# Performance work log

Hardware: AMD Instinct MI355X
Metric: run time of the kernel (lower is better)

## Reference

```python
import jax, jax.numpy as jnp
import numpy as np

N_USER, N_SPOT, D = 100000, 50000, 128
E_VISIT, E_REV, E_NEAR = 500000, 500000, 200000
P_DROP = 0.1


def _glorot(k, fan_in, fan_out):
    lim = jnp.sqrt(6.0 / (fan_in + fan_out))
    return jax.random.uniform(k, (fan_in, fan_out), jnp.float32, -lim, lim)


def setup_inputs() -> dict:
    key = jax.random.key(0)
    ks = jax.random.split(key, 14)
    return {
        "x_user": jax.random.normal(ks[0], (N_USER, D), jnp.float32),
        "x_spot": jax.random.normal(ks[1], (N_SPOT, D), jnp.float32),
        "W_visit_src": _glorot(ks[2], D, D),   # user side of (user,visit,spot)
        "W_visit_tgt": _glorot(ks[3], D, D),   # spot side of (user,visit,spot)
        "W_rev_src": _glorot(ks[4], D, D),     # spot side of (spot,visited_by,user)
        "W_rev_tgt": _glorot(ks[5], D, D),     # user side of (spot,visited_by,user)
        "W_near_src": _glorot(ks[6], D, D),    # (spot,near,spot)
        "W_near_tgt": _glorot(ks[7], D, D),
        "visit_src": jax.random.randint(ks[8], (E_VISIT,), 0, N_USER, jnp.int64),
        "visit_dst": jax.random.randint(ks[9], (E_VISIT,), 0, N_SPOT, jnp.int64),
        "rev_src": jax.random.randint(ks[10], (E_REV,), 0, N_SPOT, jnp.int64),
        "rev_dst": jax.random.randint(ks[11], (E_REV,), 0, N_USER, jnp.int64),
        "near_src": jax.random.randint(ks[12], (E_NEAR,), 0, N_SPOT, jnp.int64),
        "near_dst": jax.random.randint(ks[13], (E_NEAR,), 0, N_SPOT, jnp.int64),
    }


def _scatter_mean(vals, idx, n_seg):
    # scatter(..., reduce='mean') into zeros: empty segments stay 0
    s = jax.ops.segment_sum(vals, idx, num_segments=n_seg)
    c = jax.ops.segment_sum(jnp.ones((vals.shape[0],), vals.dtype), idx, num_segments=n_seg)
    return s / jnp.maximum(c, 1.0)[:, None]


def _edge_type(x_src, x_tgt, W_src, W_tgt, src_idx, dst_idx, n_tgt, dkey):
    src_p = x_src @ W_src                      # [N_src, D]
    tgt_p = x_tgt @ W_tgt                      # [N_tgt, D]
    g = src_p[src_idx]                         # gather per edge [E, D]
    keep = jax.random.bernoulli(dkey, 1.0 - P_DROP, g.shape)
    g = jnp.where(keep, g / (1.0 - P_DROP), jnp.zeros_like(g))  # dropout (training)
    return tgt_p + _scatter_mean(g, dst_idx, n_tgt)


def reference(x_user, x_spot, W_visit_src, W_visit_tgt, W_rev_src, W_rev_tgt,
              W_near_src, W_near_tgt, visit_src, visit_dst, rev_src, rev_dst,
              near_src, near_dst):
    dk = jax.random.key(1)
    spot_a = _edge_type(x_user, x_spot, W_visit_src, W_visit_tgt,
                        visit_src, visit_dst, N_SPOT, jax.random.fold_in(dk, 0))
    user_a = _edge_type(x_spot, x_user, W_rev_src, W_rev_tgt,
                        rev_src, rev_dst, N_USER, jax.random.fold_in(dk, 1))
    spot_b = _edge_type(x_spot, x_spot, W_near_src, W_near_tgt,
                        near_src, near_dst, N_SPOT, jax.random.fold_in(dk, 2))
    # div: spot receives from 2 edge types, user from 1
    out_user = jax.nn.relu(user_a / 1.0)
    out_spot = jax.nn.relu((spot_a + spot_b) / 2.0)
    # ReLU=True applies a second relu (no-op after the first, kept for faithfulness)
    return jax.nn.relu(out_user), jax.nn.relu(out_spot)
```

## Files before the change

### kernel.cpp

```cpp
#include <hip/hip_runtime.h>
#include <stdint.h>

#define DF 128
typedef unsigned short ushort_t;
typedef __attribute__((ext_vector_type(8))) short short8v;
typedef __attribute__((ext_vector_type(4))) float f32x4;

__host__ __device__ __forceinline__ unsigned rotl32(unsigned v, int r) {
  return __builtin_rotateleft32(v, (unsigned)r);
}

__host__ __device__ __forceinline__ void threefry2x32(
    unsigned k0, unsigned k1, unsigned c0, unsigned c1,
    unsigned& o0, unsigned& o1) {
  unsigned kx = k0 ^ k1 ^ 0x1BD11BDAu;
  unsigned x0 = c0 + k0;
  unsigned x1 = c1 + k1;
#define TF_R(r) { x0 += x1; x1 = rotl32(x1, r); x1 ^= x0; }
  TF_R(13) TF_R(15) TF_R(26) TF_R(6)
  x0 += k1; x1 += kx + 1u;
  TF_R(17) TF_R(29) TF_R(16) TF_R(24)
  x0 += kx; x1 += k0 + 2u;
  TF_R(13) TF_R(15) TF_R(26) TF_R(6)
  x0 += k0; x1 += k1 + 3u;
  TF_R(17) TF_R(29) TF_R(16) TF_R(24)
  x0 += k1; x1 += kx + 4u;
  TF_R(13) TF_R(15) TF_R(26) TF_R(6)
  x0 += kx; x1 += k0 + 5u;
#undef TF_R
  o0 = x0; o1 = x1;
}

#define KEEP_THR 0xE6666600u

__device__ __forceinline__ ushort_t f2bf(float f) {
  unsigned u = __float_as_uint(f);
  unsigned r = (u + 0x7fffu + ((u >> 16) & 1u)) >> 16;
  return (ushort_t)r;
}
__device__ __forceinline__ float bf2f(ushort_t h) {
  return __uint_as_float(((unsigned)h) << 16);
}

template <int EPI>
__global__ __launch_bounds__(256) void gemm_mfma(
    const float* __restrict__ X, const float* __restrict__ W1,
    const float* __restrict__ W2, int M,
    ushort_t* __restrict__ outB, float* __restrict__ outF,
    const ushort_t* __restrict__ m1, const ushort_t* __restrict__ m2) {
  __shared__ ushort_t Wt[DF][136];
  const int t = threadIdx.x;
  const int lane = t & 63;
  const int w = t >> 6;
  const int lr = lane & 15;
  const int kg = lane >> 4;
  const int rbase = blockIdx.x * 128;

#pragma unroll
  for (int i = 0; i < 16; ++i) {
    int q = t + i * 256;
    int k = q >> 5;
    int c4 = (q & 31) * 4;
    float4 wv = *reinterpret_cast<const float4*>(&W1[k * DF + c4]);
    if constexpr (EPI == 2) {
      float4 w2 = *reinterpret_cast<const float4*>(&W2[k * DF + c4]);
      wv.x += w2.x; wv.y += w2.y; wv.z += w2.z; wv.w += w2.w;
    }
    Wt[c4 + 0][k] = f2bf(wv.x);
    Wt[c4 + 1][k] = f2bf(wv.y);
    Wt[c4 + 2][k] = f2bf(wv.z);
    Wt[c4 + 3][k] = f2bf(wv.w);
  }
  __syncthreads();

  f32x4 acc[2][8];
#pragma unroll
  for (int rg = 0; rg < 2; ++rg)
#pragma unroll
    for (int n = 0; n < 8; ++n) acc[rg][n] = (f32x4){0.f, 0.f, 0.f, 0.f};

#pragma unroll
  for (int kt = 0; kt < 4; ++kt) {
    const int kb = kt * 32 + kg * 8;
    short8v a[2];
#pragma unroll
    for (int rg = 0; rg < 2; ++rg) {
      int r = rbase + w * 32 + rg * 16 + lr;
      float4 x0 = make_float4(0.f, 0.f, 0.f, 0.f);
      float4 x1 = x0;
      if (r < M) {
        x0 = *reinterpret_cast<const float4*>(&X[(size_t)r * DF + kb]);
        x1 = *reinterpret_cast<const float4*>(&X[(size_t)r * DF + kb + 4]);
      }
      short8v av;
      av[0] = (short)f2bf(x0.x); av[1] = (short)f2bf(x0.y);
      av[2] = (short)f2bf(x0.z); av[3] = (short)f2bf(x0.w);
      av[4] = (short)f2bf(x1.x); av[5] = (short)f2bf(x1.y);
      av[6] = (short)f2bf(x1.z); av[7] = (short)f2bf(x1.w);
      a[rg] = av;
    }
#pragma unroll
    for (int n = 0; n < 8; ++n) {
      short8v b = *reinterpret_cast<const short8v*>(&Wt[n * 16 + lr][kb]);
#pragma unroll
      for (int rg = 0; rg < 2; ++rg)
        acc[rg][n] = __builtin_amdgcn_mfma_f32_16x16x32_bf16(a[rg], b, acc[rg][n], 0, 0, 0);
    }
  }

#pragma unroll
  for (int rg = 0; rg < 2; ++rg) {
    const int rb = rbase + w * 32 + rg * 16 + kg * 4;
#pragma unroll
    for (int n = 0; n < 8; ++n) {
      const int col = n * 16 + lr;
#pragma unroll
      for (int j = 0; j < 4; ++j) {
        const int r = rb + j;
        if (r < M) {
          float vv = acc[rg][n][j];
          if (EPI == 0) {
            outB[(size_t)r * DF + col] = f2bf(vv);
          } else if (EPI == 1) {
            outF[(size_t)r * DF + col] =
                fmaxf(vv + bf2f(m1[(size_t)r * DF + col]), 0.f);
          } else {
            outF[(size_t)r * DF + col] =
                fmaxf(0.5f * (vv + bf2f(m1[(size_t)r * DF + col])
                                 + bf2f(m2[(size_t)r * DF + col])), 0.f);
          }
        }
      }
    }
  }
}

__global__ __launch_bounds__(256) void hist3(
    const int* __restrict__ vd, const int* __restrict__ rd,
    const int* __restrict__ nd, unsigned* __restrict__ deg_all,
    int Ev, int Er, int En, int segU, int segN) {
  int i = blockIdx.x * 256 + threadIdx.x;
  if (i < Ev) atomicAdd(&deg_all[vd[i]], 1u);
  else if (i < Ev + Er) atomicAdd(&deg_all[segU + rd[i - Ev]], 1u);
  else if (i < Ev + Er + En) atomicAdd(&deg_all[segN + nd[i - Ev - Er]], 1u);
}

#define SCAN_E 2048

__global__ __launch_bounds__(256) void scanA(
    const unsigned* __restrict__ deg, unsigned* __restrict__ bsum, int NT) {
  __shared__ unsigned sm[256];
  const int t = threadIdx.x;
  const int base = blockIdx.x * SCAN_E + t * 8;
  unsigned s = 0;
#pragma unroll
  for (int j = 0; j < 8; ++j) {
    int i = base + j;
    s += (i < NT) ? deg[i] : 0u;
  }
  sm[t] = s;
  __syncthreads();
  for (int off = 128; off; off >>= 1) {
    if (t < off) sm[t] += sm[t + off];
    __syncthreads();
  }
  if (t == 0) bsum[blockIdx.x] = sm[0];
}

__global__ __launch_bounds__(1024) void scanB(
    unsigned* __restrict__ bsum, unsigned* __restrict__ rp_all,
    int nb, int NT) {
  __shared__ unsigned sm[1024];
  const int t = threadIdx.x;
  unsigned v = (t < nb) ? bsum[t] : 0u;
  sm[t] = v;
  __syncthreads();
  for (int off = 1; off < 1024; off <<= 1) {
    unsigned u = (t >= off) ? sm[t - off] : 0u;
    __syncthreads();
    sm[t] += u;
    __syncthreads();
  }
  if (t < nb) bsum[t] = sm[t] - v;
  if (t == nb - 1) rp_all[NT] = sm[t];
}

__global__ __launch_bounds__(256) void scanC(
    const unsigned* __restrict__ deg, const unsigned* __restrict__ bsum,
    unsigned* __restrict__ rp, unsigned* __restrict__ cur, int NT) {
  __shared__ unsigned sm[256];
  const int t = threadIdx.x;
  const int base = blockIdx.x * SCAN_E + t * 8;
  unsigned vals[8];
  unsigned s = 0;
#pragma unroll
  for (int j = 0; j < 8; ++j) {
    int i = base + j;
    vals[j] = (i < NT) ? deg[i] : 0u;
    s += vals[j];
  }
  sm[t] = s;
  __syncthreads();
  for (int off = 1; off < 256; off <<= 1) {
    unsigned u = (t >= off) ? sm[t - off] : 0u;
    __syncthreads();
    sm[t] += u;
    __syncthreads();
  }
  unsigned run = bsum[blockIdx.x] + sm[t] - s;
#pragma unroll
  for (int j = 0; j < 8; ++j) {
    int i = base + j;
    if (i < NT) { rp[i] = run; cur[i] = run; }
    run += vals[j];
  }
}

__global__ __launch_bounds__(256) void fill3(
    const int* __restrict__ vs, const int* __restrict__ vd,
    const int* __restrict__ rs, const int* __restrict__ rd,
    const int* __restrict__ ns, const int* __restrict__ nd,
    unsigned* __restrict__ cur_all, uint2* __restrict__ es_all,
    int Ev, int Er, int En, int segU, int segN) {
  int i = blockIdx.x * 256 + threadIdx.x;
  if (i < Ev) {
    unsigned slot = atomicAdd(&cur_all[vd[i]], 1u);
    es_all[slot] = make_uint2((unsigned)i, (unsigned)vs[i]);
  } else if (i < Ev + Er) {
    int e = i - Ev;
    unsigned slot = atomicAdd(&cur_all[segU + rd[e]], 1u);
    es_all[slot] = make_uint2((unsigned)e, (unsigned)rs[e]);
  } else if (i < Ev + Er + En) {
    int e = i - Ev - Er;
    unsigned slot = atomicAdd(&cur_all[segN + nd[e]], 1u);
    es_all[slot] = make_uint2((unsigned)e, (unsigned)ns[e]);
  }
}

__global__ __launch_bounds__(256) void gather_reduce(
    const ushort_t* __restrict__ proj, const uint2* __restrict__ es,
    const unsigned* __restrict__ rowptr, ushort_t* __restrict__ accum,
    int ndst, unsigned emax, unsigned k0, unsigned k1) {
  const int lane = threadIdx.x & 63;
  int d = blockIdx.x * 4 + (threadIdx.x >> 6);
  d = __builtin_amdgcn_readfirstlane(d);
  if (d >= ndst) return;
  const unsigned b0 = __builtin_amdgcn_readfirstlane(rowptr[d]);
  const unsigned n  = __builtin_amdgcn_readfirstlane(rowptr[d + 1]) - b0;

  const unsigned lane2 = (unsigned)lane * 2u;

  uint2 e0 = es[min(b0, emax)];
  uint2 e1 = es[min(b0 + 1u, emax)];
  unsigned g0 =
      reinterpret_cast<const unsigned*>(proj + ((size_t)e0.y << 7))[lane];

  float a0 = 0.f, a1 = 0.f;
  for (unsigned i = 0; i < n; ++i) {
    const unsigned g = g0;
    const unsigned eid = e0.x;
    g0 = reinterpret_cast<const unsigned*>(proj + ((size_t)e1.y << 7))[lane];
    e0 = e1;
    e1 = es[min(b0 + i + 2u, emax)];

    const unsigned cb = eid * 128u + lane2;
    unsigned r0, r1, q0, q1;
    threefry2x32(k0, k1, 0u, cb, r0, r1);
    threefry2x32(k0, k1, 0u, cb + 1u, q0, q1);
    const float m0 = ((r0 ^ r1) < KEEP_THR) ? (1.0f / 0.9f) : 0.f;
    const float m1 = ((q0 ^ q1) < KEEP_THR) ? (1.0f / 0.9f) : 0.f;
    a0 = fmaf(__uint_as_float(g << 16), m0, a0);
    a1 = fmaf(__uint_as_float(g & 0xffff0000u), m1, a1);
  }

  const float inv = 1.0f / fmaxf((float)n, 1.0f);
  const unsigned pk =
      ((unsigned)f2bf(a0 * inv)) | (((unsigned)f2bf(a1 * inv)) << 16);
  reinterpret_cast<unsigned*>(accum)[(size_t)d * 64 + lane] = pk;
}

extern "C" void kernel_launch(void* const* d_in, const int* in_sizes, int n_in,
                              void* d_out, int out_size, void* d_ws, size_t ws_size,
                              hipStream_t stream) {
  const float* x_user      = (const float*)d_in[0];
  const float* x_spot      = (const float*)d_in[1];
  const float* W_visit_src = (const float*)d_in[2];
  const float* W_visit_tgt = (const float*)d_in[3];
  const float* W_rev_src   = (const float*)d_in[4];
  const float* W_rev_tgt   = (const float*)d_in[5];
  const float* W_near_src  = (const float*)d_in[6];
  const float* W_near_tgt  = (const float*)d_in[7];
  const int* visit_src = (const int*)d_in[8];
  const int* visit_dst = (const int*)d_in[9];
  const int* rev_src   = (const int*)d_in[10];
  const int* rev_dst   = (const int*)d_in[11];
  const int* near_src  = (const int*)d_in[12];
  const int* near_dst  = (const int*)d_in[13];

  const int n_user = in_sizes[0] / DF;
  const int n_spot = in_sizes[1] / DF;
  const int e_visit = in_sizes[8];
  const int e_rev   = in_sizes[10];
  const int e_near  = in_sizes[12];

  float* out_user = (float*)d_out;
  float* out_spot = out_user + (size_t)n_user * DF;

  const int NT = n_spot + n_user + n_spot;
  const int segU = n_spot;
  const int segN = n_spot + n_user;
  const int etot = e_visit + e_rev + e_near;
  const unsigned emax = (unsigned)(etot - 1);

  char* ws = (char*)d_ws;
  size_t off = 0;
  auto alloc = [&](size_t bytes) -> void* {
    void* p = ws + off;
    off += (bytes + 255) & ~(size_t)255;
    return p;
  };
  ushort_t* proj_vs  = (ushort_t*)alloc((size_t)n_user * DF * 2);
  ushort_t* proj_rs  = (ushort_t*)alloc((size_t)n_spot * DF * 2);
  ushort_t* proj_ns  = (ushort_t*)alloc((size_t)n_spot * DF * 2);
  ushort_t* accum_sv = (ushort_t*)alloc((size_t)n_spot * DF * 2);
  ushort_t* accum_u  = (ushort_t*)alloc((size_t)n_user * DF * 2);
  ushort_t* accum_sn = (ushort_t*)alloc((size_t)n_spot * DF * 2);
  uint2*    es_all   = (uint2*)   alloc((size_t)etot * 8);
  unsigned* rp_all   = (unsigned*)alloc(((size_t)NT + 1) * 4);
  unsigned* cur_all  = (unsigned*)alloc((size_t)NT * 4);
  unsigned* deg_all  = (unsigned*)alloc((size_t)NT * 4);
  unsigned* bsum     = (unsigned*)alloc(4096);

  unsigned kv0, kv1, kr0, kr1, kn0, kn1;
  threefry2x32(0u, 1u, 0u, 0u, kv0, kv1);
  threefry2x32(0u, 1u, 0u, 1u, kr0, kr1);
  threefry2x32(0u, 1u, 0u, 2u, kn0, kn1);

  dim3 blk(256);
  const int gb_user = (n_user + 127) / 128;
  const int gb_spot = (n_spot + 127) / 128;
  const int gb_e = (etot + 255) / 256;
  const int nb_scan = (NT + SCAN_E - 1) / SCAN_E;

  hipMemsetAsync(deg_all, 0, (size_t)NT * 4, stream);
  hist3<<<gb_e, blk, 0, stream>>>(visit_dst, rev_dst, near_dst, deg_all,
                                  e_visit, e_rev, e_near, segU, segN);
  scanA<<<nb_scan, blk, 0, stream>>>(deg_all, bsum, NT);
  scanB<<<1, 1024, 0, stream>>>(bsum, rp_all, nb_scan, NT);
  scanC<<<nb_scan, blk, 0, stream>>>(deg_all, bsum, rp_all, cur_all, NT);
  fill3<<<gb_e, blk, 0, stream>>>(visit_src, visit_dst, rev_src, rev_dst,
                                  near_src, near_dst, cur_all, es_all,
                                  e_visit, e_rev, e_near, segU, segN);

  gemm_mfma<0><<<gb_user, blk, 0, stream>>>(x_user, W_visit_src, nullptr, n_user,
                                            proj_vs, nullptr, nullptr, nullptr);
  gemm_mfma<0><<<gb_spot, blk, 0, stream>>>(x_spot, W_rev_src, nullptr, n_spot,
                                            proj_rs, nullptr, nullptr, nullptr);
  gemm_mfma<0><<<gb_spot, blk, 0, stream>>>(x_spot, W_near_src, nullptr, n_spot,
                                            proj_ns, nullptr, nullptr, nullptr);

  gather_reduce<<<(n_spot + 3) / 4, blk, 0, stream>>>(
      proj_vs, es_all, rp_all, accum_sv, n_spot, emax, kv0, kv1);
  gather_reduce<<<(n_user + 3) / 4, blk, 0, stream>>>(
      proj_rs, es_all, rp_all + segU, accum_u, n_user, emax, kr0, kr1);
  gather_reduce<<<(n_spot + 3) / 4, blk, 0, stream>>>(
      proj_ns, es_all, rp_all + segN, accum_sn, n_spot, emax, kn0, kn1);

  gemm_mfma<1><<<gb_user, blk, 0, stream>>>(x_user, W_rev_tgt, nullptr, n_user,
                                            nullptr, out_user, accum_u, nullptr);
  gemm_mfma<2><<<gb_spot, blk, 0, stream>>>(x_spot, W_visit_tgt, W_near_tgt, n_spot,
                                            nullptr, out_spot, accum_sv, accum_sn);
}
```

Baseline: 616.9 us.

## Fuse three gather-reduce launches and process two edges per wavefront iteration

Merges the three per-edge-type gather/mean kernels into one launch over all destination segments, choosing projection and RNG key per segment. Inside, each wavefront splits into two halves that each handle a different edge, with every lane loading 8 bytes and computing four threefry masks, then combining the halves with a cross-half shuffle. This halves the serial loop trip count per destination and removes launch boundaries, at the cost of more RNG work per lane per iteration and extra shuffle and select logic.

```diff
diff --git a/kernel.cpp b/kernel.cpp
--- a/kernel.cpp
+++ b/kernel.cpp
@@ -41,6 +41,9 @@
 __device__ __forceinline__ float bf2f(ushort_t h) {
   return __uint_as_float(((unsigned)h) << 16);
 }
+__device__ __forceinline__ unsigned umin_u(unsigned a, unsigned b) {
+  return a < b ? a : b;
+}
 
 template <int EPI>
 __global__ __launch_bounds__(256) void gemm_mfma(
@@ -237,46 +240,104 @@
   }
 }
 
-__global__ __launch_bounds__(256) void gather_reduce(
-    const ushort_t* __restrict__ proj, const uint2* __restrict__ es,
-    const unsigned* __restrict__ rowptr, ushort_t* __restrict__ accum,
-    int ndst, unsigned emax, unsigned k0, unsigned k1) {
+__global__ __launch_bounds__(256) void gather_reduce_all(
+    const ushort_t* __restrict__ proj_v, const ushort_t* __restrict__ proj_r,
+    const ushort_t* __restrict__ proj_n, const uint2* __restrict__ es,
+    const unsigned* __restrict__ rp, ushort_t* __restrict__ accum_all,
+    int NT, int segU, int segN, unsigned emax,
+    unsigned kv0, unsigned kv1, unsigned kr0, unsigned kr1,
+    unsigned kn0, unsigned kn1) {
   const int lane = threadIdx.x & 63;
   int d = blockIdx.x * 4 + (threadIdx.x >> 6);
   d = __builtin_amdgcn_readfirstlane(d);
-  if (d >= ndst) return;
-  const unsigned b0 = __builtin_amdgcn_readfirstlane(rowptr[d]);
-  const unsigned n  = __builtin_amdgcn_readfirstlane(rowptr[d + 1]) - b0;
-
-  const unsigned lane2 = (unsigned)lane * 2u;
-
-  uint2 e0 = es[min(b0, emax)];
-  uint2 e1 = es[min(b0 + 1u, emax)];
-  unsigned g0 =
-      reinterpret_cast<const unsigned*>(proj + ((size_t)e0.y << 7))[lane];
-
-  float a0 = 0.f, a1 = 0.f;
-  for (unsigned i = 0; i < n; ++i) {
-    const unsigned g = g0;
-    const unsigned eid = e0.x;
-    g0 = reinterpret_cast<const unsigned*>(proj + ((size_t)e1.y << 7))[lane];
-    e0 = e1;
-    e1 = es[min(b0 + i + 2u, emax)];
-
-    const unsigned cb = eid * 128u + lane2;
-    unsigned r0, r1, q0, q1;
-    threefry2x32(k0, k1, 0u, cb, r0, r1);
-    threefry2x32(k0, k1, 0u, cb + 1u, q0, q1);
-    const float m0 = ((r0 ^ r1) < KEEP_THR) ? (1.0f / 0.9f) : 0.f;
-    const float m1 = ((q0 ^ q1) < KEEP_THR) ? (1.0f / 0.9f) : 0.f;
-    a0 = fmaf(__uint_as_float(g << 16), m0, a0);
-    a1 = fmaf(__uint_as_float(g & 0xffff0000u), m1, a1);
-  }
+  if (d >= NT) return;
+
+  const ushort_t* proj;
+  unsigned k0, k1;
+  if (d < segU)      { proj = proj_v; k0 = kv0; k1 = kv1; }
+  else if (d < segN) { proj = proj_r; k0 = kr0; k1 = kr1; }
+  else               { proj = proj_n; k0 = kn0; k1 = kn1; }
+
+  const unsigned b0 = __builtin_amdgcn_readfirstlane(rp[d]);
+  const unsigned n  = __builtin_amdgcn_readfirstlane(rp[d + 1]) - b0;
+
+  const bool hi = lane >= 32;
+  const unsigned l31 = (unsigned)(lane & 31);
+  const unsigned voff8 = l31 * 8u;
+
+  const unsigned npairs = n >> 1;
+  const unsigned odd = n & 1u;
+
+  uint2 P0 = es[umin_u(b0, emax)];
+  uint2 P1 = es[umin_u(b0 + 1u, emax)];
+  unsigned eA = __builtin_amdgcn_readfirstlane(P0.x);
+  unsigned sA = __builtin_amdgcn_readfirstlane(P0.y);
+  unsigned eB = __builtin_amdgcn_readfirstlane(P1.x);
+  unsigned sB = __builtin_amdgcn_readfirstlane(P1.y);
+
+  float a0 = 0.f, a1 = 0.f, a2 = 0.f, a3 = 0.f;
+
+  for (unsigned p = 0; p < npairs; ++p) {
+    const unsigned src = hi ? sB : sA;
+    const unsigned eid = hi ? eB : eA;
+    const uint2 g = *reinterpret_cast<const uint2*>(
+        reinterpret_cast<const char*>(proj) + ((size_t)src << 8) + voff8);
+    uint2 Pn0 = es[umin_u(b0 + 2u * p + 2u, emax)];
+    uint2 Pn1 = es[umin_u(b0 + 2u * p + 3u, emax)];
+
+    const unsigned cb = eid * 128u + l31 * 4u;
+    unsigned r0a, r0b, r1a, r1b, r2a, r2b, r3a, r3b;
+    threefry2x32(k0, k1, 0u, cb + 0u, r0a, r0b);
+    threefry2x32(k0, k1, 0u, cb + 1u, r1a, r1b);
+    threefry2x32(k0, k1, 0u, cb + 2u, r2a, r2b);
+    threefry2x32(k0, k1, 0u, cb + 3u, r3a, r3b);
+    const float m0 = ((r0a ^ r0b) < KEEP_THR) ? (1.0f / 0.9f) : 0.f;
+    const float m1 = ((r1a ^ r1b) < KEEP_THR) ? (1.0f / 0.9f) : 0.f;
+    const float m2 = ((r2a ^ r2b) < KEEP_THR) ? (1.0f / 0.9f) : 0.f;
+    const float m3 = ((r3a ^ r3b) < KEEP_THR) ? (1.0f / 0.9f) : 0.f;
+    a0 = fmaf(__uint_as_float(g.x << 16), m0, a0);
+    a1 = fmaf(__uint_as_float(g.x & 0xffff0000u), m1, a1);
+    a2 = fmaf(__uint_as_float(g.y << 16), m2, a2);
+    a3 = fmaf(__uint_as_float(g.y & 0xffff0000u), m3, a3);
+
+    eA = __builtin_amdgcn_readfirstlane(Pn0.x);
+    sA = __builtin_amdgcn_readfirstlane(Pn0.y);
+    eB = __builtin_amdgcn_readfirstlane(Pn1.x);
+    sB = __builtin_amdgcn_readfirstlane(Pn1.y);
+  }
+
+  if (odd) {
+    const uint2 g = *reinterpret_cast<const uint2*>(
+        reinterpret_cast<const char*>(proj) + ((size_t)sA << 8) + voff8);
+    const unsigned cb = eA * 128u + l31 * 4u;
+    unsigned r0a, r0b, r1a, r1b, r2a, r2b, r3a, r3b;
+    threefry2x32(k0, k1, 0u, cb + 0u, r0a, r0b);
+    threefry2x32(k0, k1, 0u, cb + 1u, r1a, r1b);
+    threefry2x32(k0, k1, 0u, cb + 2u, r2a, r2b);
+    threefry2x32(k0, k1, 0u, cb + 3u, r3a, r3b);
+    const float sc = hi ? 0.f : (1.0f / 0.9f);
+    const float m0 = ((r0a ^ r0b) < KEEP_THR) ? sc : 0.f;
+    const float m1 = ((r1a ^ r1b) < KEEP_THR) ? sc : 0.f;
+    const float m2 = ((r2a ^ r2b) < KEEP_THR) ? sc : 0.f;
+    const float m3 = ((r3a ^ r3b) < KEEP_THR) ? sc : 0.f;
+    a0 = fmaf(__uint_as_float(g.x << 16), m0, a0);
+    a1 = fmaf(__uint_as_float(g.x & 0xffff0000u), m1, a1);
+    a2 = fmaf(__uint_as_float(g.y << 16), m2, a2);
+    a3 = fmaf(__uint_as_float(g.y & 0xffff0000u), m3, a3);
+  }
+
+  a0 += __shfl_xor(a0, 32);
+  a1 += __shfl_xor(a1, 32);
+  a2 += __shfl_xor(a2, 32);
+  a3 += __shfl_xor(a3, 32);
 
   const float inv = 1.0f / fmaxf((float)n, 1.0f);
+  const float u0 = hi ? a2 : a0;
+  const float u1 = hi ? a3 : a1;
   const unsigned pk =
-      ((unsigned)f2bf(a0 * inv)) | (((unsigned)f2bf(a1 * inv)) << 16);
-  reinterpret_cast<unsigned*>(accum)[(size_t)d * 64 + lane] = pk;
+      ((unsigned)f2bf(u0 * inv)) | (((unsigned)f2bf(u1 * inv)) << 16);
+  unsigned* out = reinterpret_cast<unsigned*>(accum_all) + (size_t)d * 64;
+  out[2u * l31 + (hi ? 1u : 0u)] = pk;
 }
 
 extern "C" void kernel_launch(void* const* d_in, const int* in_sizes, int n_in,
@@ -319,17 +380,19 @@
     off += (bytes + 255) & ~(size_t)255;
     return p;
   };
-  ushort_t* proj_vs  = (ushort_t*)alloc((size_t)n_user * DF * 2);
-  ushort_t* proj_rs  = (ushort_t*)alloc((size_t)n_spot * DF * 2);
-  ushort_t* proj_ns  = (ushort_t*)alloc((size_t)n_spot * DF * 2);
-  ushort_t* accum_sv = (ushort_t*)alloc((size_t)n_spot * DF * 2);
-  ushort_t* accum_u  = (ushort_t*)alloc((size_t)n_user * DF * 2);
-  ushort_t* accum_sn = (ushort_t*)alloc((size_t)n_spot * DF * 2);
-  uint2*    es_all   = (uint2*)   alloc((size_t)etot * 8);
-  unsigned* rp_all   = (unsigned*)alloc(((size_t)NT + 1) * 4);
-  unsigned* cur_all  = (unsigned*)alloc((size_t)NT * 4);
-  unsigned* deg_all  = (unsigned*)alloc((size_t)NT * 4);
-  unsigned* bsum     = (unsigned*)alloc(4096);
+  ushort_t* proj_vs   = (ushort_t*)alloc((size_t)n_user * DF * 2);
+  ushort_t* proj_rs   = (ushort_t*)alloc((size_t)n_spot * DF * 2);
+  ushort_t* proj_ns   = (ushort_t*)alloc((size_t)n_spot * DF * 2);
+  ushort_t* accum_all = (ushort_t*)alloc((size_t)NT * DF * 2);
+  uint2*    es_all    = (uint2*)   alloc((size_t)etot * 8);
+  unsigned* rp_all    = (unsigned*)alloc(((size_t)NT + 1) * 4);
+  unsigned* cur_all   = (unsigned*)alloc((size_t)NT * 4);
+  unsigned* deg_all   = (unsigned*)alloc((size_t)NT * 4);
+  unsigned* bsum      = (unsigned*)alloc(4096);
+
+  ushort_t* mean_sv = accum_all;
+  ushort_t* mean_u  = accum_all + (size_t)segU * DF;
+  ushort_t* mean_sn = accum_all + (size_t)segN * DF;
 
   unsigned kv0, kv1, kr0, kr1, kn0, kn1;
   threefry2x32(0u, 1u, 0u, 0u, kv0, kv1);
@@ -359,15 +422,12 @@
   gemm_mfma<0><<<gb_spot, blk, 0, stream>>>(x_spot, W_near_src, nullptr, n_spot,
                                             proj_ns, nullptr, nullptr, nullptr);
 
-  gather_reduce<<<(n_spot + 3) / 4, blk, 0, stream>>>(
-      proj_vs, es_all, rp_all, accum_sv, n_spot, emax, kv0, kv1);
-  gather_reduce<<<(n_user + 3) / 4, blk, 0, stream>>>(
-      proj_rs, es_all, rp_all + segU, accum_u, n_user, emax, kr0, kr1);
-  gather_reduce<<<(n_spot + 3) / 4, blk, 0, stream>>>(
-      proj_ns, es_all, rp_all + segN, accum_sn, n_spot, emax, kn0, kn1);
+  gather_reduce_all<<<(NT + 3) / 4, blk, 0, stream>>>(
+      proj_vs, proj_rs, proj_ns, es_all, rp_all, accum_all,
+      NT, segU, segN, emax, kv0, kv1, kr0, kr1, kn0, kn1);
 
   gemm_mfma<1><<<gb_user, blk, 0, stream>>>(x_user, W_rev_tgt, nullptr, n_user,
-                                            nullptr, out_user, accum_u, nullptr);
+                                            nullptr, out_user, mean_u, nullptr);
   gemm_mfma<2><<<gb_spot, blk, 0, stream>>>(x_spot, W_visit_tgt, W_near_tgt, n_spot,
-                                            nullptr, out_spot, accum_sv, accum_sn);
-}
+                                            nullptr, out_spot, mean_sv, mean_sn);
+}
```

After: 608.7 us. About the same (-1.3%).
